# Performance work log

Hardware: AMD Instinct MI355X
Metric: run time of the kernel (lower is better)

Reference implementation:

```python
import jax, jax.numpy as jnp
import numpy as np


def setup_inputs() -> dict:
    key = jax.random.key(0)
    k1, k2 = jax.random.split(key)
    x = jax.random.normal(k1, (32, 256, 56, 56), dtype=jnp.float32)
    conv_w = jax.random.normal(k2, (1, 2, 7, 7), dtype=jnp.float32) * 0.1
    return {"x": x, "conv_w": conv_w}


def reference(x, conv_w):
    # channel-wise mean and max, keepdim -> [B,1,H,W] each
    avg_out = jnp.mean(x, axis=1, keepdims=True)
    max_out = jnp.max(x, axis=1, keepdims=True)
    y = jnp.concatenate([avg_out, max_out], axis=1)  # [B,2,H,W]
    pad = (conv_w.shape[-1] - 1) // 2
    y = jax.lax.conv_general_dilated(
        y, conv_w,
        window_strides=(1, 1),
        padding=[(pad, pad), (pad, pad)],
        dimension_numbers=("NCHW", "OIHW", "NCHW"),
    )  # [B,1,H,W]
    y = jax.nn.sigmoid(y)
    return x * y
```

## Files before the change

kernel.cpp:

```cpp
#include <hip/hip_runtime.h>
#include <math.h>

#define BN   32
#define CN   256
#define HN   56
#define WN   56
#define HWN  (HN * WN)
#define CHWN (CN * HWN)
#define NPOS (BN * HWN)
#define NTOT (BN * CHWN)

__global__ void sa_reduce_kernel(const float* __restrict__ x,
                                 float* __restrict__ avg,
                                 float* __restrict__ mx) {
    int p = blockIdx.x * blockDim.x + threadIdx.x;
    if (p >= NPOS) return;
    int b = p / HWN;
    int s = p - b * HWN;
    const float* xp = x + (size_t)b * CHWN + s;
    float sum = 0.0f;
    float m = -INFINITY;
#pragma unroll 8
    for (int c = 0; c < CN; ++c) {
        float v = xp[(size_t)c * HWN];
        sum += v;
        m = fmaxf(m, v);
    }
    avg[p] = sum * (1.0f / (float)CN);
    mx[p] = m;
}

__global__ void sa_conv_kernel(const float* __restrict__ avg,
                               const float* __restrict__ mx,
                               const float* __restrict__ cw,
                               float* __restrict__ att) {
    int p = blockIdx.x * blockDim.x + threadIdx.x;
    if (p >= NPOS) return;
    int b = p / HWN;
    int s = p - b * HWN;
    int h = s / WN;
    int w = s - h * WN;
    const float* a0 = avg + b * HWN;
    const float* m0 = mx + b * HWN;
    float acc = 0.0f;
#pragma unroll
    for (int kh = 0; kh < 7; ++kh) {
        int hh = h + kh - 3;
        if (hh < 0 || hh >= HN) continue;
#pragma unroll
        for (int kw = 0; kw < 7; ++kw) {
            int ww = w + kw - 3;
            if (ww < 0 || ww >= WN) continue;
            int idx = hh * WN + ww;
            acc = fmaf(cw[kh * 7 + kw],      a0[idx], acc);
            acc = fmaf(cw[49 + kh * 7 + kw], m0[idx], acc);
        }
    }
    att[p] = 1.0f / (1.0f + expf(-acc));
}

__global__ void sa_mul_kernel(const float4* __restrict__ x4,
                              const float* __restrict__ att,
                              float4* __restrict__ out4) {
    int i = blockIdx.x * blockDim.x + threadIdx.x;
    if (i >= NTOT / 4) return;
    int e = i * 4;
    int b = e / CHWN;
    int s = e % HWN;
    const float4 a = *(const float4*)(att + b * HWN + s);
    float4 v = x4[i];
    v.x *= a.x;
    v.y *= a.y;
    v.z *= a.z;
    v.w *= a.w;
    out4[i] = v;
}

extern "C" void kernel_launch(void* const* d_in, const int* in_sizes, int n_in,
                              void* d_out, int out_size, void* d_ws, size_t ws_size,
                              hipStream_t stream) {
    const float* x  = (const float*)d_in[0];
    const float* cw = (const float*)d_in[1];
    float* out = (float*)d_out;

    float* avg = (float*)d_ws;
    float* mx  = avg + NPOS;
    float* att = mx + NPOS;

    {
        int threads = 256;
        int blocks = (NPOS + threads - 1) / threads;
        sa_reduce_kernel<<<blocks, threads, 0, stream>>>(x, avg, mx);
        sa_conv_kernel<<<blocks, threads, 0, stream>>>(avg, mx, cw, att);
    }
    {
        int n4 = NTOT / 4;
        int threads = 256;
        int blocks = (n4 + threads - 1) / threads;
        sa_mul_kernel<<<blocks, threads, 0, stream>>>((const float4*)x, att, (float4*)out);
    }
}
```

Before: 205.0 us.

## Split channel reduction across blocks and use nontemporal stores in multiply

The channel mean/max reduction is split into 8 channel chunks, each handled by separate blocks that write partial sums and maxima, followed by a small combine kernel. This raises the number of blocks in flight for the memory-bound reduction, which previously launched only NPOS/256 blocks. The multiply kernel now uses a 2D grid to drop the per-element batch division, and writes its output with nontemporal stores so the output does not pollute the cache. The cost is an extra kernel launch and extra workspace traffic for the partial results.

After: 206.6 us. No clear change (+0.8%).

```diff
diff --git a/kernel.cpp b/kernel.cpp
--- a/kernel.cpp
+++ b/kernel.cpp
@@ -1,30 +1,53 @@
 #include <hip/hip_runtime.h>
 #include <math.h>
 
-#define BN   32
-#define CN   256
-#define HN   56
-#define WN   56
-#define HWN  (HN * WN)
-#define CHWN (CN * HWN)
-#define NPOS (BN * HWN)
-#define NTOT (BN * CHWN)
+#define BN    32
+#define CN    256
+#define HN    56
+#define WN    56
+#define HWN   (HN * WN)
+#define CHWN  (CN * HWN)
+#define NPOS  (BN * HWN)
+#define NTOT  (BN * CHWN)
+#define KCH   8
+#define CPK   (CN / KCH)
+#define PBLK  (NPOS / 256)
 
-__global__ void sa_reduce_kernel(const float* __restrict__ x,
-                                 float* __restrict__ avg,
-                                 float* __restrict__ mx) {
-    int p = blockIdx.x * blockDim.x + threadIdx.x;
-    if (p >= NPOS) return;
+typedef float fx4 __attribute__((ext_vector_type(4)));
+
+__global__ void sa_reduce_part_kernel(const float* __restrict__ x,
+                                      float* __restrict__ psum,
+                                      float* __restrict__ pmax) {
+    int k = blockIdx.x / PBLK;
+    int pb = blockIdx.x - k * PBLK;
+    int p = pb * 256 + threadIdx.x;
     int b = p / HWN;
     int s = p - b * HWN;
-    const float* xp = x + (size_t)b * CHWN + s;
+    const float* xp = x + (size_t)b * CHWN + (size_t)(k * CPK) * HWN + s;
     float sum = 0.0f;
     float m = -INFINITY;
-#pragma unroll 8
-    for (int c = 0; c < CN; ++c) {
+#pragma unroll
+    for (int c = 0; c < CPK; ++c) {
         float v = xp[(size_t)c * HWN];
         sum += v;
         m = fmaxf(m, v);
+    }
+    psum[k * NPOS + p] = sum;
+    pmax[k * NPOS + p] = m;
+}
+
+__global__ void sa_combine_kernel(const float* __restrict__ psum,
+                                  const float* __restrict__ pmax,
+                                  float* __restrict__ avg,
+                                  float* __restrict__ mx) {
+    int p = blockIdx.x * blockDim.x + threadIdx.x;
+    if (p >= NPOS) return;
+    float sum = 0.0f;
+    float m = -INFINITY;
+#pragma unroll
+    for (int k = 0; k < KCH; ++k) {
+        sum += psum[k * NPOS + p];
+        m = fmaxf(m, pmax[k * NPOS + p]);
     }
     avg[p] = sum * (1.0f / (float)CN);
     mx[p] = m;
@@ -59,21 +82,18 @@
     att[p] = 1.0f / (1.0f + expf(-acc));
 }
 
-__global__ void sa_mul_kernel(const float4* __restrict__ x4,
+__global__ void sa_mul_kernel(const fx4* __restrict__ x4,
                               const float* __restrict__ att,
-                              float4* __restrict__ out4) {
+                              fx4* __restrict__ out4) {
+    int b = blockIdx.y;
     int i = blockIdx.x * blockDim.x + threadIdx.x;
-    if (i >= NTOT / 4) return;
     int e = i * 4;
-    int b = e / CHWN;
     int s = e % HWN;
-    const float4 a = *(const float4*)(att + b * HWN + s);
-    float4 v = x4[i];
-    v.x *= a.x;
-    v.y *= a.y;
-    v.z *= a.z;
-    v.w *= a.w;
-    out4[i] = v;
+    const fx4 a = *(const fx4*)(att + b * HWN + s);
+    size_t gi = (size_t)b * (CHWN / 4) + i;
+    fx4 v = x4[gi];
+    v *= a;
+    __builtin_nontemporal_store(v, &out4[gi]);
 }
 
 extern "C" void kernel_launch(void* const* d_in, const int* in_sizes, int n_in,
@@ -83,20 +103,16 @@
     const float* cw = (const float*)d_in[1];
     float* out = (float*)d_out;
 
-    float* avg = (float*)d_ws;
-    float* mx  = avg + NPOS;
-    float* att = mx + NPOS;
+    float* psum = (float*)d_ws;
+    float* pmax = psum + KCH * NPOS;
+    float* avg  = pmax + KCH * NPOS;
+    float* mx   = avg + NPOS;
+    float* att  = mx + NPOS;
 
-    {
-        int threads = 256;
-        int blocks = (NPOS + threads - 1) / threads;
-        sa_reduce_kernel<<<blocks, threads, 0, stream>>>(x, avg, mx);
-        sa_conv_kernel<<<blocks, threads, 0, stream>>>(avg, mx, cw, att);
-    }
-    {
-        int n4 = NTOT / 4;
-        int threads = 256;
-        int blocks = (n4 + threads - 1) / threads;
-        sa_mul_kernel<<<blocks, threads, 0, stream>>>((const float4*)x, att, (float4*)out);
-    }
+    sa_reduce_part_kernel<<<KCH * PBLK, 256, 0, stream>>>(x, psum, pmax);
+    sa_combine_kernel<<<PBLK, 256, 0, stream>>>(psum, pmax, avg, mx);
+    sa_conv_kernel<<<PBLK, 256, 0, stream>>>(avg, mx, cw, att);
+
+    dim3 mgrid(CHWN / 4 / 256, BN);
+    sa_mul_kernel<<<mgrid, 256, 0, stream>>>((const fx4*)x, att, (fx4*)out);
 }
```
